# Optimization experiments

Hardware: AMD Instinct MI355X
Metric: run time of the kernel (lower is better)

## Reference

```python
import jax, jax.numpy as jnp
from jax import lax
import numpy as np

B, NQ, NT = 32, 256, 512
INF = jnp.float32(1e30)  # stand-in for float('inf') mask fill; all targets are valid here
W_TRANS, W_QPOS, W_ROT = 1.0, 1.0, 1.0


def setup_inputs() -> dict:
    key = jax.random.key(0)
    k1, k2, k3, k4 = jax.random.split(key, 4)
    rot = jax.random.normal(k3, (B, NQ, 4), jnp.float32)
    rot = rot / jnp.linalg.norm(rot, axis=-1, keepdims=True)  # unit quaternions
    return {
        "translation_norm": jax.random.normal(k1, (B, NQ, 3), jnp.float32),
        "qpos_norm": jax.random.normal(k2, (B, NQ, 16), jnp.float32),
        "rotation": rot,
        "norm_pose": jax.random.normal(k4, (B, NT, 23), jnp.float32),
    }


def _l1_cost(p, t):
    # p: [B, NQ, D], t: [B, NT, D] -> [B, NQ, NT] pairwise L1
    return jnp.abs(p[:, :, None, :] - t[:, None, :, :]).sum(-1)


def _final_cost(translation_norm, qpos_norm, rotation, norm_pose):
    valid = jnp.abs(norm_pose).sum(-1) > 0  # [B, NT]
    cost = (W_TRANS * _l1_cost(translation_norm, norm_pose[..., :3])
            + W_QPOS * _l1_cost(qpos_norm, norm_pose[..., 3:19])
            + W_ROT * (1.0 - jnp.abs(jnp.einsum('bqd,bnd->bqn', rotation, norm_pose[..., 19:]))))
    return jnp.where(valid[:, None, :], cost, INF)


def _hungarian(cost):
    """Rectangular LSAP via Jonker-Volgenant shortest augmenting path
    (same algorithm as scipy.optimize.linear_sum_assignment).
    cost: [n, m] with n <= m. Returns col4row [n]: matched column per row."""
    n, m = cost.shape

    def solve_row(carry, cur_row):
        u, v, col4row, row4col = carry

        # --- Dijkstra-like search for the shortest augmenting path ---
        def s_cond(st):
            return st[6] < 0  # until a free column (sink) is found

        def s_body(st):
            i, minVal, SR, SC, spc, path, _sink = st
            SR = SR.at[i].set(True)
            r = minVal + cost[i] - u[i] - v          # reduced costs for row i
            upd = (~SC) & (r < spc)
            spc = jnp.where(upd, r, spc)
            path = jnp.where(upd, i, path)
            masked = jnp.where(SC, INF, spc)
            j = jnp.argmin(masked).astype(jnp.int32)
            minVal = masked[j]
            SC = SC.at[j].set(True)
            free = row4col[j] < 0
            sink = jnp.where(free, j, jnp.int32(-1))
            i = jnp.where(free, i, row4col[j])
            return (i, minVal, SR, SC, spc, path, sink)

        st0 = (cur_row, jnp.float32(0.0),
               jnp.zeros((n,), bool), jnp.zeros((m,), bool),
               jnp.full((m,), INF), jnp.full((m,), -1, jnp.int32), jnp.int32(-1))
        _i, minVal, SR, SC, spc, path, sink = lax.while_loop(s_cond, s_body, st0)

        # --- dual variable updates ---
        spc_row = spc[jnp.clip(col4row, 0, m - 1)]  # [n]; invalid rows masked by SR
        du = jnp.where(jnp.arange(n) == cur_row, minVal, minVal - spc_row)
        u = u + jnp.where(SR, du, 0.0)
        v = v - jnp.where(SC, minVal - spc, 0.0)

        # --- augment along the alternating path back to cur_row ---
        def a_cond(st):
            return ~st[3]

        def a_body(st):
            j, c4r, r4c, _done = st
            i = path[j]
            r4c = r4c.at[j].set(i)
            nj = c4r[i]
            c4r = c4r.at[i].set(j)
            return (nj, c4r, r4c, i == cur_row)

        _, col4row, row4col, _ = lax.while_loop(
            a_cond, a_body, (sink, col4row, row4col, False))
        return (u, v, col4row, row4col), None

    carry0 = (jnp.zeros((n,), jnp.float32), jnp.zeros((m,), jnp.float32),
              jnp.full((n,), -1, jnp.int32), jnp.full((m,), -1, jnp.int32))
    (u, v, col4row, row4col), _ = lax.scan(
        solve_row, carry0, jnp.arange(n, dtype=jnp.int32))
    return col4row


def reference(translation_norm, qpos_norm, rotation, norm_pose):
    final_cost = _final_cost(translation_norm, qpos_norm, rotation, norm_pose)
    # batched Hungarian (replaces per-batch scipy linear_sum_assignment loop)
    per_query_gt_inds = jax.vmap(_hungarian)(final_cost)        # [B, NQ]
    query_matched_mask = jnp.ones_like(per_query_gt_inds)        # all matched (NT >= NQ)
    return final_cost, per_query_gt_inds, query_matched_mask
```

## Files before the change

kernel.cpp:

```cpp
#include <hip/hip_runtime.h>

constexpr int kB  = 32;
constexpr int kNQ = 256;
constexpr int kNT = 512;
constexpr float kInf = 1e30f;
constexpr int kQTile = 32;
constexpr int kSlots = 56;
constexpr int kStride = 544;

__global__ __launch_bounds__(512)
void cost_kernel(const float* __restrict__ trans,
                 const float* __restrict__ qpos,
                 const float* __restrict__ rot,
                 const float* __restrict__ pose,
                 float* __restrict__ cost)
{
    __shared__ float sPose[kNT * 23];

    const int b     = blockIdx.x;
    const int qBase = blockIdx.y * kQTile;
    const int tid   = threadIdx.x;

    const float* pb = pose + (size_t)b * kNT * 23;
    for (int idx = tid; idx < kNT * 23; idx += 512) sPose[idx] = pb[idx];
    __syncthreads();

    float T[23];
    #pragma unroll
    for (int d = 0; d < 23; ++d) T[d] = sPose[tid * 23 + d];

    float s = 0.f;
    #pragma unroll
    for (int d = 0; d < 23; ++d) s += fabsf(T[d]);
    const bool valid = (s > 0.f);

    const float* tr = trans + ((size_t)b * kNQ + qBase) * 3;
    const float* qp = qpos  + ((size_t)b * kNQ + qBase) * 16;
    const float* rt = rot   + ((size_t)b * kNQ + qBase) * 4;
    float* cb = cost + ((size_t)b * kNQ + qBase) * kNT + tid;

    for (int q = 0; q < kQTile; ++q) {
        const float Q0 = tr[q * 3 + 0], Q1 = tr[q * 3 + 1], Q2 = tr[q * 3 + 2];
        float a = fabsf(Q0 - T[0]);
        a += fabsf(Q1 - T[1]);
        a += fabsf(Q2 - T[2]);
        float bsum = 0.f;
        #pragma unroll
        for (int d = 0; d < 16; ++d) bsum += fabsf(qp[q * 16 + d] - T[3 + d]);
        const float r0 = rt[q * 4 + 0], r1 = rt[q * 4 + 1];
        const float r2 = rt[q * 4 + 2], r3 = rt[q * 4 + 3];
        float dot = r0 * T[19] + r1 * T[20] + r2 * T[21] + r3 * T[22];
        float c = (a + bsum) + (1.0f - fabsf(dot));
        cb[(size_t)q * kNT] = valid ? c : kInf;
    }
}

__device__ __forceinline__ unsigned wave_min_u32(unsigned x) {
    unsigned t;
    t = (unsigned)__builtin_amdgcn_update_dpp((int)0xFFFFFFFF, (int)x, 0x111, 0xF, 0xF, false); x = t < x ? t : x;
    t = (unsigned)__builtin_amdgcn_update_dpp((int)0xFFFFFFFF, (int)x, 0x112, 0xF, 0xF, false); x = t < x ? t : x;
    t = (unsigned)__builtin_amdgcn_update_dpp((int)0xFFFFFFFF, (int)x, 0x114, 0xF, 0xF, false); x = t < x ? t : x;
    t = (unsigned)__builtin_amdgcn_update_dpp((int)0xFFFFFFFF, (int)x, 0x118, 0xF, 0xF, false); x = t < x ? t : x;
    t = (unsigned)__builtin_amdgcn_update_dpp((int)0xFFFFFFFF, (int)x, 0x142, 0xF, 0xF, false); x = t < x ? t : x;
    t = (unsigned)__builtin_amdgcn_update_dpp((int)0xFFFFFFFF, (int)x, 0x143, 0xF, 0xF, false); x = t < x ? t : x;
    return (unsigned)__builtin_amdgcn_readlane((int)x, 63);
}

__global__ __launch_bounds__(256)
void hungarian_kernel(const float* __restrict__ cost,
                      float* __restrict__ outInds,
                      float* __restrict__ outMask)
{
    __shared__ float rowCache[kSlots * kStride];
    __shared__ float u[kNQ];
    __shared__ int   col4row[kNQ];
    __shared__ int   row4col[kNT];
    __shared__ int   colBest[kNT];
    __shared__ int   pathL[kNT];
    __shared__ int   rowArg[kNQ];

    const int b   = blockIdx.x;
    const int tid = threadIdx.x;
    const float* __restrict__ C = cost + (size_t)b * kNQ * kNT;

    {
        const float4* Crow = (const float4*)(C + (size_t)tid * kNT);
        float bm = kInf; int barg = 0;
        #pragma unroll 4
        for (int j4 = 0; j4 < kNT / 4; ++j4) {
            float4 cc = Crow[j4];
            const int jb = j4 * 4;
            if (cc.x < bm) { bm = cc.x; barg = jb + 0; }
            if (cc.y < bm) { bm = cc.y; barg = jb + 1; }
            if (cc.z < bm) { bm = cc.z; barg = jb + 2; }
            if (cc.w < bm) { bm = cc.w; barg = jb + 3; }
        }
        u[tid]      = bm;
        rowArg[tid] = barg;
        col4row[tid] = -1;
    }
    row4col[tid] = -1;         row4col[tid + 256] = -1;
    colBest[tid] = 0x7fffffff; colBest[tid + 256] = 0x7fffffff;
    __syncthreads();
    atomicMin(&colBest[rowArg[tid]], tid);
    __syncthreads();
    {
        const int j = rowArg[tid];
        if (colBest[j] == tid) { col4row[tid] = j; row4col[j] = tid; }
    }
    __syncthreads();

    if (tid < 64) {
        const int lane = tid;
        const int laneOff = (lane >> 3) * 68 + (lane & 7) * 8;
        typedef float v2f __attribute__((ext_vector_type(2)));

        float vR[8];
        #pragma unroll
        for (int c = 0; c < 8; ++c) vR[c] = 0.f;

        int tagReg = -1;
        int rr     = 0;

        for (int cur = 0; cur < kNQ; ++cur) {
            if (col4row[cur] >= 0) continue;

            float spcR[8]; int pathR[8]; float mskA[8]; float frzV[8]; int frzP[8];
            #pragma unroll
            for (int c = 0; c < 8; ++c) {
                spcR[c] = kInf; pathR[c] = -1; mskA[c] = 0.f;
                frzV[c] = 0.f;  frzP[c] = -1;
            }
            unsigned scMask = 0;

            int   i      = cur;
            float minVal = 0.f;
            int   sink   = -1;

            for (int guard = 0; guard < kNT + 2 && sink < 0; ++guard) {
                const float ui = u[i];
                float4 p0, p1;
                const unsigned long long hm = __ballot(tagReg == i);
                if (hm != 0ull) {
                    const int slot = (int)__ffsll(hm) - 1;
                    const float4* lp = (const float4*)&rowCache[slot * kStride + laneOff];
                    p0 = lp[0]; p1 = lp[1];
                } else {
                    const float4* rp = (const float4*)(C + (size_t)i * kNT + lane * 8);
                    p0 = rp[0]; p1 = rp[1];
                    if (guard != 0) {
                        float4* wp = (float4*)&rowCache[rr * kStride + laneOff];
                        wp[0] = p0; wp[1] = p1;
                        if (lane == rr) tagReg = i;
                        rr = rr + 1; if (rr == kSlots) rr = 0;
                    }
                }

                const v2f cc2[4] = { {p0.x, p0.y}, {p0.z, p0.w},
                                     {p1.x, p1.y}, {p1.z, p1.w} };
                const v2f mv2 = { minVal, minVal };
                const v2f ui2 = { ui, ui };
                float r8[8];
                #pragma unroll
                for (int p = 0; p < 4; ++p) {
                    const v2f vv = { vR[2*p], vR[2*p + 1] };
                    const v2f rp2 = ((mv2 + cc2[p]) - ui2) - vv;
                    r8[2*p] = rp2.x; r8[2*p + 1] = rp2.y;
                }
                #pragma unroll
                for (int c = 0; c < 8; ++c) {
                    const bool lt = r8[c] < spcR[c];
                    spcR[c]  = lt ? r8[c] : spcR[c];
                    pathR[c] = lt ? i : pathR[c];
                }

                float mskv[8];
                #pragma unroll
                for (int p = 0; p < 4; ++p) {
                    const v2f s2 = { spcR[2*p], spcR[2*p + 1] };
                    const v2f a2 = { mskA[2*p], mskA[2*p + 1] };
                    const v2f m2 = s2 + a2;
                    mskv[2*p] = m2.x; mskv[2*p + 1] = m2.y;
                }
                unsigned sp[8];
                #pragma unroll
                for (int c = 0; c < 8; ++c) sp[c] = __float_as_uint(mskv[c]);
                unsigned mA = sp[1] < sp[0] ? sp[1] : sp[0]; int aA = sp[1] < sp[0] ? 1 : 0;
                unsigned mB = sp[3] < sp[2] ? sp[3] : sp[2]; int aB = sp[3] < sp[2] ? 3 : 2;
                unsigned mC = sp[5] < sp[4] ? sp[5] : sp[4]; int aC = sp[5] < sp[4] ? 5 : 4;
                unsigned mD = sp[7] < sp[6] ? sp[7] : sp[6]; int aD = sp[7] < sp[6] ? 7 : 6;
                unsigned mAB = mB < mA ? mB : mA; int aAB = mB < mA ? aB : aA;
                unsigned mCD = mD < mC ? mD : mC; int aCD = mD < mC ? aD : aC;
                unsigned lvu = mCD < mAB ? mCD : mAB; int lc = mCD < mAB ? aCD : aAB;
                const int lix  = lane * 8 + lc;
                const int spec = row4col[lix];

                const unsigned gmu = wave_min_u32(lvu);
                const unsigned long long bal = __ballot(lvu == gmu);
                const int wl    = (int)__ffsll(bal) - 1;
                const int jstar = __builtin_amdgcn_readlane(lix, wl);
                const int own   = __builtin_amdgcn_readlane(spec, wl);
                minVal = __uint_as_float(gmu);

                if (own < 0) sink = jstar;
                else         i    = own;

                if (wl == lane) {
                    const int lcw = jstar & 7;
                    scMask |= 1u << lcw;
                    #pragma unroll
                    for (int c = 0; c < 8; ++c) {
                        if (c == lcw) {
                            mskA[c] = __builtin_inff();
                            frzV[c] = minVal;
                            frzP[c] = pathR[c];
                        }
                    }
                }
            }

            if (lane == 0) u[cur] += minVal;
            #pragma unroll
            for (int c = 0; c < 8; ++c) {
                if ((scMask >> c) & 1u) {
                    const int j = lane * 8 + c;
                    const int r = row4col[j];
                    const float d = minVal - frzV[c];
                    if (r >= 0) u[r] += d;
                    vR[c] -= d;
                    pathL[j] = frzP[c];
                }
            }
            __threadfence_block();

            if (lane == 0 && sink >= 0) {
                int j = sink;
                while (true) {
                    const int pi = pathL[j];
                    row4col[j] = pi;
                    const int nj = col4row[pi];
                    col4row[pi] = j;
                    if (pi == cur) break;
                    j = nj;
                }
            }
            __threadfence_block();
        }
    }
    __syncthreads();

    outInds[(size_t)b * kNQ + tid] = (float)col4row[tid];
    outMask[(size_t)b * kNQ + tid] = 1.0f;
}

extern "C" void kernel_launch(void* const* d_in, const int* in_sizes, int n_in,
                              void* d_out, int out_size, void* d_ws, size_t ws_size,
                              hipStream_t stream) {
    const float* trans = (const float*)d_in[0];
    const float* qpos  = (const float*)d_in[1];
    const float* rot   = (const float*)d_in[2];
    const float* pose  = (const float*)d_in[3];

    float* out  = (float*)d_out;
    float* cost = out;
    float* inds = out + (size_t)kB * kNQ * kNT;
    float* mask = inds + (size_t)kB * kNQ;

    dim3 g1(kB, kNQ / kQTile);
    cost_kernel<<<g1, 512, 0, stream>>>(trans, qpos, rot, pose, cost);
    hungarian_kernel<<<kB, 256, 0, stream>>>(cost, inds, mask);
}
```

Measured before the change: 432.7 us.

## Interleave two Hungarian problems per wave to hide row-load latency

Each block now solves two batch items with one wave, alternating Dijkstra steps between them. The next row load is issued at the end of a step and consumed on the following tick, so one problem's global load latency overlaps the other's compute. Free rows are gathered into a compacted list up front, and the per-problem row cache shrinks to fit LDS. The grid is halved to 16 blocks, which reduces parallelism across CUs and can serialize work if the two problems need different numbers of steps.

```diff
diff --git a/kernel.cpp b/kernel.cpp
--- a/kernel.cpp
+++ b/kernel.cpp
@@ -5,7 +5,7 @@
 constexpr int kNT = 512;
 constexpr float kInf = 1e30f;
 constexpr int kQTile = 32;
-constexpr int kSlots = 56;
+constexpr int kSlots = 30;
 constexpr int kStride = 544;
 
 __global__ __launch_bounds__(512)
@@ -71,186 +71,235 @@
                       float* __restrict__ outInds,
                       float* __restrict__ outMask)
 {
-    __shared__ float rowCache[kSlots * kStride];
-    __shared__ float u[kNQ];
-    __shared__ int   col4row[kNQ];
-    __shared__ int   row4col[kNT];
-    __shared__ int   colBest[kNT];
-    __shared__ int   pathL[kNT];
-    __shared__ int   rowArg[kNQ];
-
-    const int b   = blockIdx.x;
+    __shared__ float rowCache[2][kSlots * kStride];
+    __shared__ float u[2][kNQ];
+    __shared__ int   col4row[2][kNQ];
+    __shared__ int   row4col[2][kNT];
+    __shared__ int   pathL[2][kNT];
+    __shared__ int   colBest[2][kNT];
+    __shared__ int   rowArg[2][kNQ];
+    __shared__ int   freeList[2][kNQ];
+    __shared__ unsigned long long fmask[2][4];
+    __shared__ int   nFreeS[2];
+
+    const int blk = blockIdx.x;
     const int tid = threadIdx.x;
-    const float* __restrict__ C = cost + (size_t)b * kNQ * kNT;
-
-    {
-        const float4* Crow = (const float4*)(C + (size_t)tid * kNT);
-        float bm = kInf; int barg = 0;
-        #pragma unroll 4
-        for (int j4 = 0; j4 < kNT / 4; ++j4) {
-            float4 cc = Crow[j4];
-            const int jb = j4 * 4;
-            if (cc.x < bm) { bm = cc.x; barg = jb + 0; }
-            if (cc.y < bm) { bm = cc.y; barg = jb + 1; }
-            if (cc.z < bm) { bm = cc.z; barg = jb + 2; }
-            if (cc.w < bm) { bm = cc.w; barg = jb + 3; }
+    const int wv  = tid >> 6, ln = tid & 63;
+
+    for (int s = 0; s < 2; ++s) {
+        const float* C = cost + (size_t)(blk * 2 + s) * kNQ * kNT;
+        {
+            const float4* Crow = (const float4*)(C + (size_t)tid * kNT);
+            float bm = kInf; int barg = 0;
+            #pragma unroll 4
+            for (int j4 = 0; j4 < kNT / 4; ++j4) {
+                float4 cc = Crow[j4];
+                const int jb = j4 * 4;
+                if (cc.x < bm) { bm = cc.x; barg = jb + 0; }
+                if (cc.y < bm) { bm = cc.y; barg = jb + 1; }
+                if (cc.z < bm) { bm = cc.z; barg = jb + 2; }
+                if (cc.w < bm) { bm = cc.w; barg = jb + 3; }
+            }
+            u[s][tid] = bm;
+            rowArg[s][tid] = barg;
+            col4row[s][tid] = -1;
         }
-        u[tid]      = bm;
-        rowArg[tid] = barg;
-        col4row[tid] = -1;
+        row4col[s][tid] = -1;           row4col[s][tid + 256] = -1;
+        colBest[s][tid] = 0x7fffffff;   colBest[s][tid + 256] = 0x7fffffff;
+        __syncthreads();
+        atomicMin(&colBest[s][rowArg[s][tid]], tid);
+        __syncthreads();
+        {
+            const int j = rowArg[s][tid];
+            if (colBest[s][j] == tid) { col4row[s][tid] = j; row4col[s][j] = tid; }
+        }
+        __syncthreads();
+        {
+            const bool f = col4row[s][tid] < 0;
+            const unsigned long long m = __ballot(f);
+            if (ln == 0) fmask[s][wv] = m;
+            __syncthreads();
+            int base = 0;
+            for (int w = 0; w < wv; ++w) base += __popcll(fmask[s][w]);
+            if (f) freeList[s][base + __popcll(m & ((1ull << ln) - 1ull))] = tid;
+            if (tid == 0)
+                nFreeS[s] = __popcll(fmask[s][0]) + __popcll(fmask[s][1])
+                          + __popcll(fmask[s][2]) + __popcll(fmask[s][3]);
+            __syncthreads();
+        }
     }
-    row4col[tid] = -1;         row4col[tid + 256] = -1;
-    colBest[tid] = 0x7fffffff; colBest[tid + 256] = 0x7fffffff;
-    __syncthreads();
-    atomicMin(&colBest[rowArg[tid]], tid);
-    __syncthreads();
-    {
-        const int j = rowArg[tid];
-        if (colBest[j] == tid) { col4row[tid] = j; row4col[j] = tid; }
-    }
-    __syncthreads();
 
     if (tid < 64) {
         const int lane = tid;
         const int laneOff = (lane >> 3) * 68 + (lane & 7) * 8;
         typedef float v2f __attribute__((ext_vector_type(2)));
 
-        float vR[8];
+        const float* Cb[2] = { cost + (size_t)(blk * 2 + 0) * kNQ * kNT,
+                               cost + (size_t)(blk * 2 + 1) * kNQ * kNT };
+
+        float vRa[2][8], spc[2][8], mskA[2][8], frzV[2][8];
+        int   pth[2][8], frzP[2][8];
+        unsigned scM[2];
+        int   tag[2] = { -1, -1 }, rr[2] = { 0, 0 };
+        bool  pend[2] = { false, false };
+        int   pendSlot[2] = { 0, 0 };
+        float4 pA[2], pB[2];
+        float uiC[2];
+        bool done[2] = { false, false }, act[2] = { false, false };
+        int  frI[2] = { 0, 0 }, curR[2] = { -1, -1 }, iR[2] = { -1, -1 };
+        float mvR[2] = { 0.f, 0.f };
+        const int nF[2] = { nFreeS[0], nFreeS[1] };
         #pragma unroll
-        for (int c = 0; c < 8; ++c) vR[c] = 0.f;
-
-        int tagReg = -1;
-        int rr     = 0;
-
-        for (int cur = 0; cur < kNQ; ++cur) {
-            if (col4row[cur] >= 0) continue;
-
-            float spcR[8]; int pathR[8]; float mskA[8]; float frzV[8]; int frzP[8];
+        for (int c = 0; c < 8; ++c) { vRa[0][c] = 0.f; vRa[1][c] = 0.f; }
+
+        auto issue = [&](int s, int i, bool allowIns) {
+            uiC[s] = u[s][i];
+            const unsigned long long hm = __ballot(tag[s] == i);
+            if (hm != 0ull) {
+                const int slot = (int)__ffsll(hm) - 1;
+                const float4* lp = (const float4*)&rowCache[s][slot * kStride + laneOff];
+                pA[s] = lp[0]; pB[s] = lp[1];
+            } else {
+                const float4* rp = (const float4*)(Cb[s] + (size_t)i * kNT + lane * 8);
+                pA[s] = rp[0]; pB[s] = rp[1];
+                if (allowIns) {
+                    pend[s] = true; pendSlot[s] = rr[s];
+                    if (lane == rr[s]) tag[s] = i;
+                    rr[s] = rr[s] + 1; if (rr[s] == kSlots) rr[s] = 0;
+                }
+            }
+        };
+
+        auto start = [&](int s) {
+            if (frI[s] >= nF[s]) { done[s] = true; return; }
+            curR[s] = freeList[s][frI[s]++];
             #pragma unroll
             for (int c = 0; c < 8; ++c) {
-                spcR[c] = kInf; pathR[c] = -1; mskA[c] = 0.f;
-                frzV[c] = 0.f;  frzP[c] = -1;
-            }
-            unsigned scMask = 0;
-
-            int   i      = cur;
-            float minVal = 0.f;
-            int   sink   = -1;
-
-            for (int guard = 0; guard < kNT + 2 && sink < 0; ++guard) {
-                const float ui = u[i];
-                float4 p0, p1;
-                const unsigned long long hm = __ballot(tagReg == i);
-                if (hm != 0ull) {
-                    const int slot = (int)__ffsll(hm) - 1;
-                    const float4* lp = (const float4*)&rowCache[slot * kStride + laneOff];
-                    p0 = lp[0]; p1 = lp[1];
-                } else {
-                    const float4* rp = (const float4*)(C + (size_t)i * kNT + lane * 8);
-                    p0 = rp[0]; p1 = rp[1];
-                    if (guard != 0) {
-                        float4* wp = (float4*)&rowCache[rr * kStride + laneOff];
-                        wp[0] = p0; wp[1] = p1;
-                        if (lane == rr) tagReg = i;
-                        rr = rr + 1; if (rr == kSlots) rr = 0;
+                spc[s][c] = kInf; pth[s][c] = -1; mskA[s][c] = 0.f;
+                frzV[s][c] = 0.f; frzP[s][c] = -1;
+            }
+            scM[s] = 0; mvR[s] = 0.f; iR[s] = curR[s];
+            issue(s, iR[s], false);
+            act[s] = true;
+        };
+
+        auto step = [&](int s) {
+            if (pend[s]) {
+                float4* wp = (float4*)&rowCache[s][pendSlot[s] * kStride + laneOff];
+                wp[0] = pA[s]; wp[1] = pB[s];
+                pend[s] = false;
+            }
+            const float4 p0 = pA[s], p1 = pB[s];
+            const float ui = uiC[s];
+            const float minVal = mvR[s];
+            const int   i = iR[s];
+
+            const v2f cc2[4] = { {p0.x, p0.y}, {p0.z, p0.w},
+                                 {p1.x, p1.y}, {p1.z, p1.w} };
+            const v2f mv2 = { minVal, minVal };
+            const v2f ui2 = { ui, ui };
+            float r8[8];
+            #pragma unroll
+            for (int p = 0; p < 4; ++p) {
+                const v2f vv = { vRa[s][2*p], vRa[s][2*p + 1] };
+                const v2f rp2 = ((mv2 + cc2[p]) - ui2) - vv;
+                r8[2*p] = rp2.x; r8[2*p + 1] = rp2.y;
+            }
+            #pragma unroll
+            for (int c = 0; c < 8; ++c) {
+                const bool lt = r8[c] < spc[s][c];
+                spc[s][c] = lt ? r8[c] : spc[s][c];
+                pth[s][c] = lt ? i : pth[s][c];
+            }
+
+            float mskv[8];
+            #pragma unroll
+            for (int p = 0; p < 4; ++p) {
+                const v2f s2 = { spc[s][2*p], spc[s][2*p + 1] };
+                const v2f a2 = { mskA[s][2*p], mskA[s][2*p + 1] };
+                const v2f m2 = s2 + a2;
+                mskv[2*p] = m2.x; mskv[2*p + 1] = m2.y;
+            }
+            unsigned sp[8];
+            #pragma unroll
+            for (int c = 0; c < 8; ++c) sp[c] = __float_as_uint(mskv[c]);
+            unsigned mA = sp[1] < sp[0] ? sp[1] : sp[0]; int aA = sp[1] < sp[0] ? 1 : 0;
+            unsigned mB = sp[3] < sp[2] ? sp[3] : sp[2]; int aB = sp[3] < sp[2] ? 3 : 2;
+            unsigned mC = sp[5] < sp[4] ? sp[5] : sp[4]; int aC = sp[5] < sp[4] ? 5 : 4;
+            unsigned mD = sp[7] < sp[6] ? sp[7] : sp[6]; int aD = sp[7] < sp[6] ? 7 : 6;
+            unsigned mAB = mB < mA ? mB : mA; int aAB = mB < mA ? aB : aA;
+            unsigned mCD = mD < mC ? mD : mC; int aCD = mD < mC ? aD : aC;
+            unsigned lvu = mCD < mAB ? mCD : mAB; int lc = mCD < mAB ? aCD : aAB;
+            const int lix  = lane * 8 + lc;
+            const int spec = row4col[s][lix];
+
+            const unsigned gmu = wave_min_u32(lvu);
+            const unsigned long long bal = __ballot(lvu == gmu);
+            const int wl    = (int)__ffsll(bal) - 1;
+            const int jstar = __builtin_amdgcn_readlane(lix, wl);
+            const int own   = __builtin_amdgcn_readlane(spec, wl);
+            const float mv  = __uint_as_float(gmu);
+            mvR[s] = mv;
+
+            if (wl == lane) {
+                const int lcw = jstar & 7;
+                scM[s] |= 1u << lcw;
+                #pragma unroll
+                for (int c = 0; c < 8; ++c) {
+                    if (c == lcw) {
+                        mskA[s][c] = __builtin_inff();
+                        frzV[s][c] = mv;
+                        frzP[s][c] = pth[s][c];
                     }
                 }
-
-                const v2f cc2[4] = { {p0.x, p0.y}, {p0.z, p0.w},
-                                     {p1.x, p1.y}, {p1.z, p1.w} };
-                const v2f mv2 = { minVal, minVal };
-                const v2f ui2 = { ui, ui };
-                float r8[8];
-                #pragma unroll
-                for (int p = 0; p < 4; ++p) {
-                    const v2f vv = { vR[2*p], vR[2*p + 1] };
-                    const v2f rp2 = ((mv2 + cc2[p]) - ui2) - vv;
-                    r8[2*p] = rp2.x; r8[2*p + 1] = rp2.y;
-                }
+            }
+
+            if (own < 0) {
+                if (lane == 0) u[s][curR[s]] += mv;
                 #pragma unroll
                 for (int c = 0; c < 8; ++c) {
-                    const bool lt = r8[c] < spcR[c];
-                    spcR[c]  = lt ? r8[c] : spcR[c];
-                    pathR[c] = lt ? i : pathR[c];
-                }
-
-                float mskv[8];
-                #pragma unroll
-                for (int p = 0; p < 4; ++p) {
-                    const v2f s2 = { spcR[2*p], spcR[2*p + 1] };
-                    const v2f a2 = { mskA[2*p], mskA[2*p + 1] };
-                    const v2f m2 = s2 + a2;
-                    mskv[2*p] = m2.x; mskv[2*p + 1] = m2.y;
-                }
-                unsigned sp[8];
-                #pragma unroll
-                for (int c = 0; c < 8; ++c) sp[c] = __float_as_uint(mskv[c]);
-                unsigned mA = sp[1] < sp[0] ? sp[1] : sp[0]; int aA = sp[1] < sp[0] ? 1 : 0;
-                unsigned mB = sp[3] < sp[2] ? sp[3] : sp[2]; int aB = sp[3] < sp[2] ? 3 : 2;
-                unsigned mC = sp[5] < sp[4] ? sp[5] : sp[4]; int aC = sp[5] < sp[4] ? 5 : 4;
-                unsigned mD = sp[7] < sp[6] ? sp[7] : sp[6]; int aD = sp[7] < sp[6] ? 7 : 6;
-                unsigned mAB = mB < mA ? mB : mA; int aAB = mB < mA ? aB : aA;
-                unsigned mCD = mD < mC ? mD : mC; int aCD = mD < mC ? aD : aC;
-                unsigned lvu = mCD < mAB ? mCD : mAB; int lc = mCD < mAB ? aCD : aAB;
-                const int lix  = lane * 8 + lc;
-                const int spec = row4col[lix];
-
-                const unsigned gmu = wave_min_u32(lvu);
-                const unsigned long long bal = __ballot(lvu == gmu);
-                const int wl    = (int)__ffsll(bal) - 1;
-                const int jstar = __builtin_amdgcn_readlane(lix, wl);
-                const int own   = __builtin_amdgcn_readlane(spec, wl);
-                minVal = __uint_as_float(gmu);
-
-                if (own < 0) sink = jstar;
-                else         i    = own;
-
-                if (wl == lane) {
-                    const int lcw = jstar & 7;
-                    scMask |= 1u << lcw;
-                    #pragma unroll
-                    for (int c = 0; c < 8; ++c) {
-                        if (c == lcw) {
-                            mskA[c] = __builtin_inff();
-                            frzV[c] = minVal;
-                            frzP[c] = pathR[c];
-                        }
+                    if ((scM[s] >> c) & 1u) {
+                        const int j = lane * 8 + c;
+                        const int r = row4col[s][j];
+                        const float d = mv - frzV[s][c];
+                        if (r >= 0) u[s][r] += d;
+                        vRa[s][c] -= d;
+                        pathL[s][j] = frzP[s][c];
                     }
                 }
-            }
-
-            if (lane == 0) u[cur] += minVal;
-            #pragma unroll
-            for (int c = 0; c < 8; ++c) {
-                if ((scMask >> c) & 1u) {
-                    const int j = lane * 8 + c;
-                    const int r = row4col[j];
-                    const float d = minVal - frzV[c];
-                    if (r >= 0) u[r] += d;
-                    vR[c] -= d;
-                    pathL[j] = frzP[c];
+                __threadfence_block();
+                if (lane == 0) {
+                    int j = jstar;
+                    while (true) {
+                        const int pi = pathL[s][j];
+                        row4col[s][j] = pi;
+                        const int nj = col4row[s][pi];
+                        col4row[s][pi] = j;
+                        if (pi == curR[s]) break;
+                        j = nj;
+                    }
                 }
-            }
-            __threadfence_block();
-
-            if (lane == 0 && sink >= 0) {
-                int j = sink;
-                while (true) {
-                    const int pi = pathL[j];
-                    row4col[j] = pi;
-                    const int nj = col4row[pi];
-                    col4row[pi] = j;
-                    if (pi == cur) break;
-                    j = nj;
-                }
-            }
-            __threadfence_block();
+                __threadfence_block();
+                act[s] = false;
+            } else {
+                iR[s] = own;
+                issue(s, own, true);
+            }
+        };
+
+        for (int tick = 0; tick < 400000 && !(done[0] && done[1]); ++tick) {
+            if (!done[0]) { if (!act[0]) start(0); else step(0); }
+            if (!done[1]) { if (!act[1]) start(1); else step(1); }
         }
     }
     __syncthreads();
 
-    outInds[(size_t)b * kNQ + tid] = (float)col4row[tid];
-    outMask[(size_t)b * kNQ + tid] = 1.0f;
+    #pragma unroll
+    for (int s = 0; s < 2; ++s) {
+        const int b = blk * 2 + s;
+        outInds[(size_t)b * kNQ + tid] = (float)col4row[s][tid];
+        outMask[(size_t)b * kNQ + tid] = 1.0f;
+    }
 }
 
 extern "C" void kernel_launch(void* const* d_in, const int* in_sizes, int n_in,
@@ -268,5 +317,5 @@
 
     dim3 g1(kB, kNQ / kQTile);
     cost_kernel<<<g1, 512, 0, stream>>>(trans, qpos, rot, pose, cost);
-    hungarian_kernel<<<kB, 256, 0, stream>>>(cost, inds, mask);
+    hungarian_kernel<<<kB / 2, 256, 0, stream>>>(cost, inds, mask);
 }
```

After: 995.7 us. 2.3x slower.

## Pack eight batch Hungarian solves per block and drop LDS row cache

Applied to the files above, without the earlier changes.

The Hungarian kernel now runs eight batches per 512-thread block, one wavefront per batch, with per-wave shared-memory state, instead of one batch per 256-thread block with a single active wave. The LDS row cache for cost rows is removed, and every Dijkstra step reads its cost row straight from global memory (L2). This cuts the block count from 32 to 4, so each block holds eight independent serial solvers. The risk is that all 32 waves land on only 4 CUs, that every row fetch pays global-memory latency instead of an LDS hit, and that the initial per-row argmin is done by 64 threads per batch instead of 256.

```diff
diff --git a/kernel.cpp b/kernel.cpp
--- a/kernel.cpp
+++ b/kernel.cpp
@@ -5,8 +5,7 @@
 constexpr int kNT = 512;
 constexpr float kInf = 1e30f;
 constexpr int kQTile = 32;
-constexpr int kSlots = 56;
-constexpr int kStride = 544;
+constexpr int kWPB   = 8;
 
 __global__ __launch_bounds__(512)
 void cost_kernel(const float* __restrict__ trans,
@@ -66,25 +65,28 @@
     return (unsigned)__builtin_amdgcn_readlane((int)x, 63);
 }
 
-__global__ __launch_bounds__(256)
+__global__ __launch_bounds__(512)
 void hungarian_kernel(const float* __restrict__ cost,
                       float* __restrict__ outInds,
                       float* __restrict__ outMask)
 {
-    __shared__ float rowCache[kSlots * kStride];
-    __shared__ float u[kNQ];
-    __shared__ int   col4row[kNQ];
-    __shared__ int   row4col[kNT];
-    __shared__ int   colBest[kNT];
-    __shared__ int   pathL[kNT];
-    __shared__ int   rowArg[kNQ];
-
-    const int b   = blockIdx.x;
-    const int tid = threadIdx.x;
+    __shared__ float u[kWPB][kNQ];
+    __shared__ int   col4row[kWPB][kNQ];
+    __shared__ int   row4col[kWPB][kNT];
+    __shared__ int   pathL[kWPB][kNT];
+    __shared__ int   colBest[kWPB][kNT];
+    __shared__ int   rowArg[kWPB][kNQ];
+
+    const int tid  = threadIdx.x;
+    const int w    = tid >> 6;
+    const int lane = tid & 63;
+    const int b    = blockIdx.x * kWPB + w;
     const float* __restrict__ C = cost + (size_t)b * kNQ * kNT;
 
-    {
-        const float4* Crow = (const float4*)(C + (size_t)tid * kNT);
+    #pragma unroll
+    for (int k = 0; k < 4; ++k) {
+        const int r = lane * 4 + k;
+        const float4* Crow = (const float4*)(C + (size_t)r * kNT);
         float bm = kInf; int barg = 0;
         #pragma unroll 4
         for (int j4 = 0; j4 < kNT / 4; ++j4) {
@@ -95,35 +97,38 @@
             if (cc.z < bm) { bm = cc.z; barg = jb + 2; }
             if (cc.w < bm) { bm = cc.w; barg = jb + 3; }
         }
-        u[tid]      = bm;
-        rowArg[tid] = barg;
-        col4row[tid] = -1;
-    }
-    row4col[tid] = -1;         row4col[tid + 256] = -1;
-    colBest[tid] = 0x7fffffff; colBest[tid + 256] = 0x7fffffff;
-    __syncthreads();
-    atomicMin(&colBest[rowArg[tid]], tid);
-    __syncthreads();
+        u[w][r] = bm;
+        rowArg[w][r] = barg;
+        col4row[w][r] = -1;
+    }
+    #pragma unroll
+    for (int k = 0; k < 8; ++k) {
+        row4col[w][lane * 8 + k] = -1;
+        colBest[w][lane * 8 + k] = 0x7fffffff;
+    }
+    __syncthreads();
+    #pragma unroll
+    for (int k = 0; k < 4; ++k) {
+        const int r = lane * 4 + k;
+        atomicMin(&colBest[w][rowArg[w][r]], r);
+    }
+    __syncthreads();
+    #pragma unroll
+    for (int k = 0; k < 4; ++k) {
+        const int r = lane * 4 + k;
+        const int j = rowArg[w][r];
+        if (colBest[w][j] == r) { col4row[w][r] = j; row4col[w][j] = r; }
+    }
+    __syncthreads();
+
     {
-        const int j = rowArg[tid];
-        if (colBest[j] == tid) { col4row[tid] = j; row4col[j] = tid; }
-    }
-    __syncthreads();
-
-    if (tid < 64) {
-        const int lane = tid;
-        const int laneOff = (lane >> 3) * 68 + (lane & 7) * 8;
         typedef float v2f __attribute__((ext_vector_type(2)));
-
         float vR[8];
         #pragma unroll
         for (int c = 0; c < 8; ++c) vR[c] = 0.f;
 
-        int tagReg = -1;
-        int rr     = 0;
-
         for (int cur = 0; cur < kNQ; ++cur) {
-            if (col4row[cur] >= 0) continue;
+            if (col4row[w][cur] >= 0) continue;
 
             float spcR[8]; int pathR[8]; float mskA[8]; float frzV[8]; int frzP[8];
             #pragma unroll
@@ -138,23 +143,9 @@
             int   sink   = -1;
 
             for (int guard = 0; guard < kNT + 2 && sink < 0; ++guard) {
-                const float ui = u[i];
-                float4 p0, p1;
-                const unsigned long long hm = __ballot(tagReg == i);
-                if (hm != 0ull) {
-                    const int slot = (int)__ffsll(hm) - 1;
-                    const float4* lp = (const float4*)&rowCache[slot * kStride + laneOff];
-                    p0 = lp[0]; p1 = lp[1];
-                } else {
-                    const float4* rp = (const float4*)(C + (size_t)i * kNT + lane * 8);
-                    p0 = rp[0]; p1 = rp[1];
-                    if (guard != 0) {
-                        float4* wp = (float4*)&rowCache[rr * kStride + laneOff];
-                        wp[0] = p0; wp[1] = p1;
-                        if (lane == rr) tagReg = i;
-                        rr = rr + 1; if (rr == kSlots) rr = 0;
-                    }
-                }
+                const float ui = u[w][i];
+                const float4* rp = (const float4*)(C + (size_t)i * kNT + lane * 8);
+                const float4 p0 = rp[0], p1 = rp[1];
 
                 const v2f cc2[4] = { {p0.x, p0.y}, {p0.z, p0.w},
                                      {p1.x, p1.y}, {p1.z, p1.w} };
@@ -193,7 +184,7 @@
                 unsigned mCD = mD < mC ? mD : mC; int aCD = mD < mC ? aD : aC;
                 unsigned lvu = mCD < mAB ? mCD : mAB; int lc = mCD < mAB ? aCD : aAB;
                 const int lix  = lane * 8 + lc;
-                const int spec = row4col[lix];
+                const int spec = row4col[w][lix];
 
                 const unsigned gmu = wave_min_u32(lvu);
                 const unsigned long long bal = __ballot(lvu == gmu);
@@ -219,16 +210,16 @@
                 }
             }
 
-            if (lane == 0) u[cur] += minVal;
+            if (lane == 0) u[w][cur] += minVal;
             #pragma unroll
             for (int c = 0; c < 8; ++c) {
                 if ((scMask >> c) & 1u) {
                     const int j = lane * 8 + c;
-                    const int r = row4col[j];
+                    const int r = row4col[w][j];
                     const float d = minVal - frzV[c];
-                    if (r >= 0) u[r] += d;
+                    if (r >= 0) u[w][r] += d;
                     vR[c] -= d;
-                    pathL[j] = frzP[c];
+                    pathL[w][j] = frzP[c];
                 }
             }
             __threadfence_block();
@@ -236,10 +227,10 @@
             if (lane == 0 && sink >= 0) {
                 int j = sink;
                 while (true) {
-                    const int pi = pathL[j];
-                    row4col[j] = pi;
-                    const int nj = col4row[pi];
-                    col4row[pi] = j;
+                    const int pi = pathL[w][j];
+                    row4col[w][j] = pi;
+                    const int nj = col4row[w][pi];
+                    col4row[w][pi] = j;
                     if (pi == cur) break;
                     j = nj;
                 }
@@ -247,10 +238,13 @@
             __threadfence_block();
         }
     }
-    __syncthreads();
-
-    outInds[(size_t)b * kNQ + tid] = (float)col4row[tid];
-    outMask[(size_t)b * kNQ + tid] = 1.0f;
+
+    #pragma unroll
+    for (int k = 0; k < 4; ++k) {
+        const int r = lane * 4 + k;
+        outInds[(size_t)b * kNQ + r] = (float)col4row[w][r];
+        outMask[(size_t)b * kNQ + r] = 1.0f;
+    }
 }
 
 extern "C" void kernel_launch(void* const* d_in, const int* in_sizes, int n_in,
@@ -268,5 +262,5 @@
 
     dim3 g1(kB, kNQ / kQTile);
     cost_kernel<<<g1, 512, 0, stream>>>(trans, qpos, rot, pose, cost);
-    hungarian_kernel<<<kB, 256, 0, stream>>>(cost, inds, mask);
-}
+    hungarian_kernel<<<kB / kWPB, 512, 0, stream>>>(cost, inds, mask);
+}
```

Measured after the change: 571.2 us. 32.0% more time.
